# Performance work log

Hardware: AMD Instinct MI355X
Metric: run time of the kernel (lower is better)

## Reference

```python
import jax, jax.numpy as jnp
import numpy as np

B, T = 64, 512
L, D = 2048, 512


def setup_inputs() -> dict:
    key = jax.random.key(0)
    k1, k2, k3 = jax.random.split(key, 3)
    label_sequences = jax.random.randint(k1, (B, T), 0, L)
    source_embeddings = jax.random.normal(k2, (L, D), dtype=jnp.float32)
    target_embeddings = jax.random.normal(k3, (L, D), dtype=jnp.float32)
    return {
        "label_sequences": label_sequences,
        "source_embeddings": source_embeddings,
        "target_embeddings": target_embeddings,
    }


def reference(label_sequences, source_embeddings, target_embeddings):
    # source_index = labels[:, :-1], target_index = labels[:, 1:]
    src_idx = label_sequences[:, :-1]          # [B, T-1]
    tgt_idx = label_sequences[:, 1:]           # [B, T-1]
    # Gather source embeddings per transition pair: [B, T-1, D]
    src = source_embeddings[src_idx]
    # Logits over all target labels: [B, T-1, L]
    logits = jnp.einsum("btd,ld->btl", src, target_embeddings)
    # Row-wise log_softmax over target labels (dim=1 in torch == last axis here)
    logp = jax.nn.log_softmax(logits, axis=-1)
    # Pick the actual next label's log-probability: [B, T-1]
    scores = jnp.take_along_axis(logp, tgt_idx[..., None], axis=-1)[..., 0]
    return scores
```

## Files before the change

kernel.cpp:

```cpp
#include <hip/hip_runtime.h>
#include <hip/hip_bf16.h>

#define L_CLS 2048
#define D_DIM 512
#define T_SZ  512
#define NT    511
#define NOUT  (64 * NT)
#define NCHUNK 32
#define LDS_STRIDE 136
#define LOG2E 1.4426950408889634f
#define LN2   0.6931471805599453f
#define SHIFT 128.0f

typedef __attribute__((ext_vector_type(8))) short bf16x8;
typedef __attribute__((ext_vector_type(4))) float f32x4;

static __device__ __forceinline__ short f2bf(float x) {
    return (short)__bfloat16_as_ushort(__float2bfloat16(x));
}

__launch_bounds__(256)
__global__ void gemm_lse(const float* __restrict__ srcE,
                         const float* __restrict__ tgtE,
                         float* __restrict__ psum,
                         float* __restrict__ M, int useM) {
    __shared__ __hip_bfloat16 Blds[64 * LDS_STRIDE];

    const int tid  = threadIdx.x;
    const int wave = tid >> 6;
    const int lane = tid & 63;
    const int lr   = lane & 15;
    const int hi   = lane >> 4;
    const int by   = blockIdx.y;
    const int C    = by * 64;
    const int R0   = blockIdx.x * 64 + wave * 16;
    const int R1   = (blockIdx.x + 16) * 64 + wave * 16;

    f32x4 acc[2][4];
#pragma unroll
    for (int rb = 0; rb < 2; ++rb)
#pragma unroll
        for (int ct = 0; ct < 4; ++ct) acc[rb][ct] = (f32x4){0.f, 0.f, 0.f, 0.f};

#pragma unroll
    for (int s = 0; s < 4; ++s) {
#pragma unroll
        for (int i = 0; i < 4; ++i) {
            int p   = tid + 256 * i;
            int row = p >> 4;
            int grp = p & 15;
            const f32x4* g = reinterpret_cast<const f32x4*>(
                tgtE + (C + row) * D_DIM + s * 128 + grp * 8);
            f32x4 x0 = g[0], x1 = g[1];
            bf16x8 w;
#pragma unroll
            for (int e = 0; e < 4; ++e) { w[e] = f2bf(x0[e]); w[e + 4] = f2bf(x1[e]); }
            *reinterpret_cast<bf16x8*>(&Blds[row * LDS_STRIDE + grp * 8]) = w;
        }
        __syncthreads();

#pragma unroll
        for (int rb = 0; rb < 2; ++rb) {
            const int R = rb ? R1 : R0;
            bf16x8 a[4];
            const float* arow = srcE + (R + lr) * D_DIM + s * 128 + hi * 8;
#pragma unroll
            for (int ks = 0; ks < 4; ++ks) {
                const f32x4* g = reinterpret_cast<const f32x4*>(arow + ks * 32);
                f32x4 x0 = g[0], x1 = g[1];
                bf16x8 v;
#pragma unroll
                for (int e = 0; e < 4; ++e) { v[e] = f2bf(x0[e]); v[e + 4] = f2bf(x1[e]); }
                a[ks] = v;
            }
#pragma unroll
            for (int ks = 0; ks < 4; ++ks) {
                const int off = ks * 32 + hi * 8;
#pragma unroll
                for (int ct = 0; ct < 4; ++ct) {
                    bf16x8 b = *reinterpret_cast<const bf16x8*>(
                        &Blds[(ct * 16 + lr) * LDS_STRIDE + off]);
                    acc[rb][ct] = __builtin_amdgcn_mfma_f32_16x16x32_bf16(
                        a[ks], b, acc[rb][ct], 0, 0, 0);
                }
            }
        }
        __syncthreads();
    }

#pragma unroll
    for (int rb = 0; rb < 2; ++rb) {
        const int R = rb ? R1 : R0;
        if (useM) {
#pragma unroll
            for (int i = 0; i < 4; ++i) {
                size_t rg = (size_t)(R + hi * 4 + i) * L_CLS + C + lr;
                M[rg]      = acc[rb][0][i];
                M[rg + 16] = acc[rb][1][i];
                M[rg + 32] = acc[rb][2][i];
                M[rg + 48] = acc[rb][3][i];
            }
        }
        float p[4];
#pragma unroll
        for (int i = 0; i < 4; ++i) {
            p[i] = exp2f(acc[rb][0][i] * LOG2E - SHIFT)
                 + exp2f(acc[rb][1][i] * LOG2E - SHIFT)
                 + exp2f(acc[rb][2][i] * LOG2E - SHIFT)
                 + exp2f(acc[rb][3][i] * LOG2E - SHIFT);
        }
#pragma unroll
        for (int off = 1; off < 16; off <<= 1)
#pragma unroll
            for (int i = 0; i < 4; ++i) p[i] += __shfl_xor(p[i], off);
        if (lr == 0) {
#pragma unroll
            for (int i = 0; i < 4; ++i)
                psum[(R + hi * 4 + i) * NCHUNK + by] = p[i];
        }
    }
}

__launch_bounds__(256)
__global__ void scores_gather(const int* __restrict__ labels,
                              const float* __restrict__ psum,
                              const float* __restrict__ M,
                              float* __restrict__ out) {
    int o = blockIdx.x * 256 + threadIdx.x;
    if (o >= NOUT) return;
    int b = o / NT;
    int t = o - b * NT;
    int src = labels[b * T_SZ + t];
    int tgt = labels[b * T_SZ + t + 1];

    const f32x4* p4 = reinterpret_cast<const f32x4*>(psum) + src * (NCHUNK / 4);
    f32x4 sv = {0.f, 0.f, 0.f, 0.f};
#pragma unroll
    for (int c = 0; c < NCHUNK / 4; ++c) {
        f32x4 v = p4[c];
        sv[0] += v[0]; sv[1] += v[1]; sv[2] += v[2]; sv[3] += v[3];
    }
    float S = (sv[0] + sv[1]) + (sv[2] + sv[3]);
    float lse = (log2f(S) + SHIFT) * LN2;
    out[o] = M[(size_t)src * L_CLS + tgt] - lse;
}

__launch_bounds__(256)
__global__ void scores_dot(const int* __restrict__ labels,
                           const float* __restrict__ srcE,
                           const float* __restrict__ tgtE,
                           const float* __restrict__ psum,
                           float* __restrict__ out) {
    const int wid  = blockIdx.x * 4 + (threadIdx.x >> 6);
    const int lane = threadIdx.x & 63;
    const int b = wid / NT;
    const int t = wid - b * NT;
    const int src = labels[b * T_SZ + t];
    const int tgt = labels[b * T_SZ + t + 1];

    const f32x4* sp = reinterpret_cast<const f32x4*>(srcE + src * D_DIM + lane * 8);
    const f32x4* tp = reinterpret_cast<const f32x4*>(tgtE + tgt * D_DIM + lane * 8);
    f32x4 s0 = sp[0], s1 = sp[1];
    f32x4 t0 = tp[0], t1 = tp[1];
    float acc = 0.f;
#pragma unroll
    for (int j = 0; j < 4; ++j) acc += s0[j] * t0[j] + s1[j] * t1[j];
    float ps = (lane < NCHUNK) ? psum[src * NCHUNK + lane] : 0.f;
#pragma unroll
    for (int off = 32; off; off >>= 1) {
        acc += __shfl_xor(acc, off);
        ps  += __shfl_xor(ps, off);
    }
    if (lane == 0) out[wid] = acc - (log2f(ps) + SHIFT) * LN2;
}

extern "C" void kernel_launch(void* const* d_in, const int* in_sizes, int n_in,
                              void* d_out, int out_size, void* d_ws, size_t ws_size,
                              hipStream_t stream) {
    const int*   labels = (const int*)d_in[0];
    const float* srcE   = (const float*)d_in[1];
    const float* tgtE   = (const float*)d_in[2];
    float*       out    = (float*)d_out;

    float* psum = (float*)d_ws;
    float* M    = psum + L_CLS * NCHUNK;

    size_t need = ((size_t)L_CLS * NCHUNK + (size_t)L_CLS * L_CLS) * sizeof(float);
    int useM = (ws_size >= need) ? 1 : 0;

    gemm_lse<<<dim3(16, NCHUNK), 256, 0, stream>>>(srcE, tgtE, psum, M, useM);
    if (useM)
        scores_gather<<<(NOUT + 255) / 256, 256, 0, stream>>>(labels, psum, M, out);
    else
        scores_dot<<<NOUT / 4, 256, 0, stream>>>(labels, srcE, tgtE, psum, out);
}
```

Before: 31.79 us.

## Widen GEMM column tile to 128 and share B fragments across row blocks

Doubles each block's target-label tile from 64 to 128 columns, halving the number of column chunks and partial sums. Each LDS B fragment is now reused for both row blocks in one interleaved MFMA loop. The grid is transposed so blockIdx.x indexes column chunks, the s-loop is no longer unrolled, and the psum reduction is simplified to 16 entries. This cuts repeated conversion of A and fewer psum reads, but uses more accumulator registers and LDS while halving the grid to 256 blocks, which may underfill the GPU.

```diff
diff --git a/kernel.cpp b/kernel.cpp
--- a/kernel.cpp
+++ b/kernel.cpp
@@ -6,7 +6,7 @@
 #define T_SZ  512
 #define NT    511
 #define NOUT  (64 * NT)
-#define NCHUNK 32
+#define NCHUNK 16
 #define LDS_STRIDE 136
 #define LOG2E 1.4426950408889634f
 #define LN2   0.6931471805599453f
@@ -24,45 +24,46 @@
                          const float* __restrict__ tgtE,
                          float* __restrict__ psum,
                          float* __restrict__ M, int useM) {
-    __shared__ __hip_bfloat16 Blds[64 * LDS_STRIDE];
+    __shared__ __hip_bfloat16 Blds[128 * LDS_STRIDE];
 
     const int tid  = threadIdx.x;
     const int wave = tid >> 6;
     const int lane = tid & 63;
     const int lr   = lane & 15;
     const int hi   = lane >> 4;
-    const int by   = blockIdx.y;
-    const int C    = by * 64;
-    const int R0   = blockIdx.x * 64 + wave * 16;
-    const int R1   = (blockIdx.x + 16) * 64 + wave * 16;
+    const int by   = blockIdx.x;
+    const int bx   = blockIdx.y;
+    const int C    = by * 128;
+    const int R0   = bx * 64 + wave * 16;
+    const int R1   = (bx + 16) * 64 + wave * 16;
 
-    f32x4 acc[2][4];
+    f32x4 acc[2][8];
 #pragma unroll
     for (int rb = 0; rb < 2; ++rb)
 #pragma unroll
-        for (int ct = 0; ct < 4; ++ct) acc[rb][ct] = (f32x4){0.f, 0.f, 0.f, 0.f};
+        for (int ct = 0; ct < 8; ++ct) acc[rb][ct] = (f32x4){0.f, 0.f, 0.f, 0.f};
 
-#pragma unroll
+#pragma unroll 1
     for (int s = 0; s < 4; ++s) {
 #pragma unroll
-        for (int i = 0; i < 4; ++i) {
+        for (int i = 0; i < 8; ++i) {
             int p   = tid + 256 * i;
             int row = p >> 4;
             int grp = p & 15;
             const f32x4* g = reinterpret_cast<const f32x4*>(
                 tgtE + (C + row) * D_DIM + s * 128 + grp * 8);
             f32x4 x0 = g[0], x1 = g[1];
-            bf16x8 w;
+            bf16x8 v;
 #pragma unroll
-            for (int e = 0; e < 4; ++e) { w[e] = f2bf(x0[e]); w[e + 4] = f2bf(x1[e]); }
-            *reinterpret_cast<bf16x8*>(&Blds[row * LDS_STRIDE + grp * 8]) = w;
+            for (int e = 0; e < 4; ++e) { v[e] = f2bf(x0[e]); v[e + 4] = f2bf(x1[e]); }
+            *reinterpret_cast<bf16x8*>(&Blds[row * LDS_STRIDE + grp * 8]) = v;
         }
         __syncthreads();
 
+        bf16x8 a[2][4];
 #pragma unroll
         for (int rb = 0; rb < 2; ++rb) {
             const int R = rb ? R1 : R0;
-            bf16x8 a[4];
             const float* arow = srcE + (R + lr) * D_DIM + s * 128 + hi * 8;
 #pragma unroll
             for (int ks = 0; ks < 4; ++ks) {
@@ -71,18 +72,19 @@
                 bf16x8 v;
 #pragma unroll
                 for (int e = 0; e < 4; ++e) { v[e] = f2bf(x0[e]); v[e + 4] = f2bf(x1[e]); }
-                a[ks] = v;
+                a[rb][ks] = v;
             }
+        }
+
 #pragma unroll
-            for (int ks = 0; ks < 4; ++ks) {
-                const int off = ks * 32 + hi * 8;
+        for (int ks = 0; ks < 4; ++ks) {
+            const int off = ks * 32 + hi * 8;
 #pragma unroll
-                for (int ct = 0; ct < 4; ++ct) {
-                    bf16x8 b = *reinterpret_cast<const bf16x8*>(
-                        &Blds[(ct * 16 + lr) * LDS_STRIDE + off]);
-                    acc[rb][ct] = __builtin_amdgcn_mfma_f32_16x16x32_bf16(
-                        a[ks], b, acc[rb][ct], 0, 0, 0);
-                }
+            for (int ct = 0; ct < 8; ++ct) {
+                bf16x8 b = *reinterpret_cast<const bf16x8*>(
+                    &Blds[(ct * 16 + lr) * LDS_STRIDE + off]);
+                acc[0][ct] = __builtin_amdgcn_mfma_f32_16x16x32_bf16(a[0][ks], b, acc[0][ct], 0, 0, 0);
+                acc[1][ct] = __builtin_amdgcn_mfma_f32_16x16x32_bf16(a[1][ks], b, acc[1][ct], 0, 0, 0);
             }
         }
         __syncthreads();
@@ -95,19 +97,18 @@
 #pragma unroll
             for (int i = 0; i < 4; ++i) {
                 size_t rg = (size_t)(R + hi * 4 + i) * L_CLS + C + lr;
-                M[rg]      = acc[rb][0][i];
-                M[rg + 16] = acc[rb][1][i];
-                M[rg + 32] = acc[rb][2][i];
-                M[rg + 48] = acc[rb][3][i];
+#pragma unroll
+                for (int ct = 0; ct < 8; ++ct)
+                    M[rg + ct * 16] = acc[rb][ct][i];
             }
         }
         float p[4];
 #pragma unroll
         for (int i = 0; i < 4; ++i) {
-            p[i] = exp2f(acc[rb][0][i] * LOG2E - SHIFT)
-                 + exp2f(acc[rb][1][i] * LOG2E - SHIFT)
-                 + exp2f(acc[rb][2][i] * LOG2E - SHIFT)
-                 + exp2f(acc[rb][3][i] * LOG2E - SHIFT);
+            p[i] = 0.f;
+#pragma unroll
+            for (int ct = 0; ct < 8; ++ct)
+                p[i] += exp2f(acc[rb][ct][i] * LOG2E - SHIFT);
         }
 #pragma unroll
         for (int off = 1; off < 16; off <<= 1)
@@ -133,14 +134,10 @@
     int src = labels[b * T_SZ + t];
     int tgt = labels[b * T_SZ + t + 1];
 
-    const f32x4* p4 = reinterpret_cast<const f32x4*>(psum) + src * (NCHUNK / 4);
-    f32x4 sv = {0.f, 0.f, 0.f, 0.f};
-#pragma unroll
-    for (int c = 0; c < NCHUNK / 4; ++c) {
-        f32x4 v = p4[c];
-        sv[0] += v[0]; sv[1] += v[1]; sv[2] += v[2]; sv[3] += v[3];
-    }
-    float S = (sv[0] + sv[1]) + (sv[2] + sv[3]);
+    const f32x4* pv = reinterpret_cast<const f32x4*>(psum + src * NCHUNK);
+    f32x4 s0 = pv[0], s1 = pv[1], s2 = pv[2], s3 = pv[3];
+    float S = (s0[0]+s0[1]+s0[2]+s0[3]) + (s1[0]+s1[1]+s1[2]+s1[3])
+            + (s2[0]+s2[1]+s2[2]+s2[3]) + (s3[0]+s3[1]+s3[2]+s3[3]);
     float lse = (log2f(S) + SHIFT) * LN2;
     out[o] = M[(size_t)src * L_CLS + tgt] - lse;
 }
@@ -188,7 +185,7 @@
     size_t need = ((size_t)L_CLS * NCHUNK + (size_t)L_CLS * L_CLS) * sizeof(float);
     int useM = (ws_size >= need) ? 1 : 0;
 
-    gemm_lse<<<dim3(16, NCHUNK), 256, 0, stream>>>(srcE, tgtE, psum, M, useM);
+    gemm_lse<<<dim3(NCHUNK, 16), 256, 0, stream>>>(srcE, tgtE, psum, M, useM);
     if (useM)
         scores_gather<<<(NOUT + 255) / 256, 256, 0, stream>>>(labels, psum, M, out);
     else
```

Measured after the change: 31.62 us. About the same (-0.5%).

## Pre-convert tables to bf16 and use double-buffered 32x32 MFMA GEMM tiles

Applied to the files above, without the earlier changes.

Adds a separate kernel that converts both embedding tables to bf16 once, so the GEMM no longer converts fp32 to bf16 inside its inner loop. The GEMM moves to 128x128 tiles with 512 threads, 32x32x16 MFMA instructions, register prefetch of the next K slice and double-buffered LDS. The scores_dot fallback path and the workspace-size check are removed, so the full logit matrix is always materialised. This adds an extra launch and a bf16 round trip through memory, and assumes the workspace is large enough.

```diff
diff --git a/kernel.cpp b/kernel.cpp
--- a/kernel.cpp
+++ b/kernel.cpp
@@ -7,116 +7,136 @@
 #define NT    511
 #define NOUT  (64 * NT)
 #define NCHUNK 32
-#define LDS_STRIDE 136
+#define LDSS  136
 #define LOG2E 1.4426950408889634f
 #define LN2   0.6931471805599453f
 #define SHIFT 128.0f
 
-typedef __attribute__((ext_vector_type(8))) short bf16x8;
-typedef __attribute__((ext_vector_type(4))) float f32x4;
+typedef __attribute__((ext_vector_type(8)))  short bf16x8;
+typedef __attribute__((ext_vector_type(4)))  float f32x4;
+typedef __attribute__((ext_vector_type(16))) float f32x16;
 
 static __device__ __forceinline__ short f2bf(float x) {
     return (short)__bfloat16_as_ushort(__float2bfloat16(x));
 }
 
-__launch_bounds__(256)
-__global__ void gemm_lse(const float* __restrict__ srcE,
-                         const float* __restrict__ tgtE,
-                         float* __restrict__ psum,
-                         float* __restrict__ M, int useM) {
-    __shared__ __hip_bfloat16 Blds[64 * LDS_STRIDE];
+__global__ void conv_bf16(const float* __restrict__ srcE, const float* __restrict__ tgtE,
+                          __hip_bfloat16* __restrict__ Sb, __hip_bfloat16* __restrict__ Tb) {
+    int i = blockIdx.x * blockDim.x + threadIdx.x;
+    if (i >= (L_CLS * D_DIM) / 8) return;
+    const f32x4* s4 = reinterpret_cast<const f32x4*>(srcE) + i * 2;
+    const f32x4* t4 = reinterpret_cast<const f32x4*>(tgtE) + i * 2;
+    f32x4 s0 = s4[0], s1 = s4[1];
+    f32x4 t0 = t4[0], t1 = t4[1];
+    bf16x8 so, to;
+#pragma unroll
+    for (int j = 0; j < 4; ++j) {
+        so[j] = f2bf(s0[j]); so[j + 4] = f2bf(s1[j]);
+        to[j] = f2bf(t0[j]); to[j + 4] = f2bf(t1[j]);
+    }
+    reinterpret_cast<bf16x8*>(Sb)[i] = so;
+    reinterpret_cast<bf16x8*>(Tb)[i] = to;
+}
+
+__launch_bounds__(512, 1)
+__global__ void gemm_lse_bf16(const __hip_bfloat16* __restrict__ Sb,
+                              const __hip_bfloat16* __restrict__ Tb,
+                              float* __restrict__ psum,
+                              float* __restrict__ M) {
+    __shared__ __hip_bfloat16 Blds[2][128 * LDSS];
 
     const int tid  = threadIdx.x;
     const int wave = tid >> 6;
     const int lane = tid & 63;
-    const int lr   = lane & 15;
-    const int hi   = lane >> 4;
-    const int by   = blockIdx.y;
-    const int C    = by * 64;
-    const int R0   = blockIdx.x * 64 + wave * 16;
-    const int R1   = (blockIdx.x + 16) * 64 + wave * 16;
+    const int l31  = lane & 31;
+    const int hk   = lane >> 5;
+    const int rs   = (wave & 3) * 32;
+    const int chf  = wave >> 2;
+    const int C    = blockIdx.x * 128;
+    const int Rb   = blockIdx.y * 128;
+    const int Ar   = Rb + rs + l31;
 
-    f32x4 acc[2][4];
+    f32x16 acc0, acc1;
 #pragma unroll
-    for (int rb = 0; rb < 2; ++rb)
+    for (int r = 0; r < 16; ++r) { acc0[r] = 0.f; acc1[r] = 0.f; }
+
+    bf16x8 stg[4], an[8];
 #pragma unroll
-        for (int ct = 0; ct < 4; ++ct) acc[rb][ct] = (f32x4){0.f, 0.f, 0.f, 0.f};
+    for (int i = 0; i < 4; ++i) {
+        int p = tid + 512 * i;
+        stg[i] = *reinterpret_cast<const bf16x8*>(
+            &Tb[(C + (p >> 4)) * D_DIM + (p & 15) * 8]);
+    }
+#pragma unroll
+    for (int ks = 0; ks < 8; ++ks)
+        an[ks] = *reinterpret_cast<const bf16x8*>(
+            &Sb[Ar * D_DIM + ks * 16 + hk * 8]);
+#pragma unroll
+    for (int i = 0; i < 4; ++i) {
+        int p = tid + 512 * i;
+        *reinterpret_cast<bf16x8*>(&Blds[0][(p >> 4) * LDSS + (p & 15) * 8]) = stg[i];
+    }
+    __syncthreads();
 
 #pragma unroll
     for (int s = 0; s < 4; ++s) {
+        const int cur = s & 1;
+        bf16x8 a[8];
 #pragma unroll
-        for (int i = 0; i < 4; ++i) {
-            int p   = tid + 256 * i;
-            int row = p >> 4;
-            int grp = p & 15;
-            const f32x4* g = reinterpret_cast<const f32x4*>(
-                tgtE + (C + row) * D_DIM + s * 128 + grp * 8);
-            f32x4 x0 = g[0], x1 = g[1];
-            bf16x8 w;
+        for (int ks = 0; ks < 8; ++ks) a[ks] = an[ks];
+
+        if (s < 3) {
 #pragma unroll
-            for (int e = 0; e < 4; ++e) { w[e] = f2bf(x0[e]); w[e + 4] = f2bf(x1[e]); }
-            *reinterpret_cast<bf16x8*>(&Blds[row * LDS_STRIDE + grp * 8]) = w;
-        }
-        __syncthreads();
-
-#pragma unroll
-        for (int rb = 0; rb < 2; ++rb) {
-            const int R = rb ? R1 : R0;
-            bf16x8 a[4];
-            const float* arow = srcE + (R + lr) * D_DIM + s * 128 + hi * 8;
-#pragma unroll
-            for (int ks = 0; ks < 4; ++ks) {
-                const f32x4* g = reinterpret_cast<const f32x4*>(arow + ks * 32);
-                f32x4 x0 = g[0], x1 = g[1];
-                bf16x8 v;
-#pragma unroll
-                for (int e = 0; e < 4; ++e) { v[e] = f2bf(x0[e]); v[e + 4] = f2bf(x1[e]); }
-                a[ks] = v;
+            for (int i = 0; i < 4; ++i) {
+                int p = tid + 512 * i;
+                stg[i] = *reinterpret_cast<const bf16x8*>(
+                    &Tb[(C + (p >> 4)) * D_DIM + (s + 1) * 128 + (p & 15) * 8]);
             }
 #pragma unroll
-            for (int ks = 0; ks < 4; ++ks) {
-                const int off = ks * 32 + hi * 8;
+            for (int ks = 0; ks < 8; ++ks)
+                an[ks] = *reinterpret_cast<const bf16x8*>(
+                    &Sb[Ar * D_DIM + (s + 1) * 128 + ks * 16 + hk * 8]);
+        }
+
+        const __hip_bfloat16* Bb = Blds[cur];
 #pragma unroll
-                for (int ct = 0; ct < 4; ++ct) {
-                    bf16x8 b = *reinterpret_cast<const bf16x8*>(
-                        &Blds[(ct * 16 + lr) * LDS_STRIDE + off]);
-                    acc[rb][ct] = __builtin_amdgcn_mfma_f32_16x16x32_bf16(
-                        a[ks], b, acc[rb][ct], 0, 0, 0);
-                }
+        for (int ks = 0; ks < 8; ++ks) {
+            const int off = ks * 16 + hk * 8;
+            bf16x8 b0 = *reinterpret_cast<const bf16x8*>(&Bb[(chf * 64 + l31) * LDSS + off]);
+            bf16x8 b1 = *reinterpret_cast<const bf16x8*>(&Bb[(chf * 64 + 32 + l31) * LDSS + off]);
+            acc0 = __builtin_amdgcn_mfma_f32_32x32x16_bf16(a[ks], b0, acc0, 0, 0, 0);
+            acc1 = __builtin_amdgcn_mfma_f32_32x32x16_bf16(a[ks], b1, acc1, 0, 0, 0);
+        }
+
+        if (s < 3) {
+#pragma unroll
+            for (int i = 0; i < 4; ++i) {
+                int p = tid + 512 * i;
+                *reinterpret_cast<bf16x8*>(
+                    &Blds[cur ^ 1][(p >> 4) * LDSS + (p & 15) * 8]) = stg[i];
             }
+            __syncthreads();
         }
-        __syncthreads();
     }
 
+    float p[16];
 #pragma unroll
-    for (int rb = 0; rb < 2; ++rb) {
-        const int R = rb ? R1 : R0;
-        if (useM) {
+    for (int r = 0; r < 16; ++r) {
+        int grow = Rb + rs + (r & 3) + 8 * (r >> 2) + 4 * hk;
+        size_t base = (size_t)grow * L_CLS + C + chf * 64 + l31;
+        M[base]      = acc0[r];
+        M[base + 32] = acc1[r];
+        p[r] = exp2f(acc0[r] * LOG2E - SHIFT) + exp2f(acc1[r] * LOG2E - SHIFT);
+    }
 #pragma unroll
-            for (int i = 0; i < 4; ++i) {
-                size_t rg = (size_t)(R + hi * 4 + i) * L_CLS + C + lr;
-                M[rg]      = acc[rb][0][i];
-                M[rg + 16] = acc[rb][1][i];
-                M[rg + 32] = acc[rb][2][i];
-                M[rg + 48] = acc[rb][3][i];
-            }
-        }
-        float p[4];
+    for (int off = 1; off < 32; off <<= 1)
 #pragma unroll
-        for (int i = 0; i < 4; ++i) {
-            p[i] = exp2f(acc[rb][0][i] * LOG2E - SHIFT)
-                 + exp2f(acc[rb][1][i] * LOG2E - SHIFT)
-                 + exp2f(acc[rb][2][i] * LOG2E - SHIFT)
-                 + exp2f(acc[rb][3][i] * LOG2E - SHIFT);
-        }
+        for (int r = 0; r < 16; ++r) p[r] += __shfl_xor(p[r], off);
+    if (l31 == 0) {
 #pragma unroll
-        for (int off = 1; off < 16; off <<= 1)
-#pragma unroll
-            for (int i = 0; i < 4; ++i) p[i] += __shfl_xor(p[i], off);
-        if (lr == 0) {
-#pragma unroll
-            for (int i = 0; i < 4; ++i)
-                psum[(R + hi * 4 + i) * NCHUNK + by] = p[i];
+        for (int r = 0; r < 16; ++r) {
+            int grow = Rb + rs + (r & 3) + 8 * (r >> 2) + 4 * hk;
+            psum[grow * NCHUNK + blockIdx.x * 2 + chf] = p[r];
         }
     }
 }
@@ -133,45 +153,16 @@
     int src = labels[b * T_SZ + t];
     int tgt = labels[b * T_SZ + t + 1];
 
-    const f32x4* p4 = reinterpret_cast<const f32x4*>(psum) + src * (NCHUNK / 4);
-    f32x4 sv = {0.f, 0.f, 0.f, 0.f};
+    const f32x4* pv = reinterpret_cast<const f32x4*>(psum + src * NCHUNK);
+    f32x4 sv = pv[0];
 #pragma unroll
-    for (int c = 0; c < NCHUNK / 4; ++c) {
-        f32x4 v = p4[c];
+    for (int c = 1; c < NCHUNK / 4; ++c) {
+        f32x4 v = pv[c];
         sv[0] += v[0]; sv[1] += v[1]; sv[2] += v[2]; sv[3] += v[3];
     }
     float S = (sv[0] + sv[1]) + (sv[2] + sv[3]);
     float lse = (log2f(S) + SHIFT) * LN2;
     out[o] = M[(size_t)src * L_CLS + tgt] - lse;
-}
-
-__launch_bounds__(256)
-__global__ void scores_dot(const int* __restrict__ labels,
-                           const float* __restrict__ srcE,
-                           const float* __restrict__ tgtE,
-                           const float* __restrict__ psum,
-                           float* __restrict__ out) {
-    const int wid  = blockIdx.x * 4 + (threadIdx.x >> 6);
-    const int lane = threadIdx.x & 63;
-    const int b = wid / NT;
-    const int t = wid - b * NT;
-    const int src = labels[b * T_SZ + t];
-    const int tgt = labels[b * T_SZ + t + 1];
-
-    const f32x4* sp = reinterpret_cast<const f32x4*>(srcE + src * D_DIM + lane * 8);
-    const f32x4* tp = reinterpret_cast<const f32x4*>(tgtE + tgt * D_DIM + lane * 8);
-    f32x4 s0 = sp[0], s1 = sp[1];
-    f32x4 t0 = tp[0], t1 = tp[1];
-    float acc = 0.f;
-#pragma unroll
-    for (int j = 0; j < 4; ++j) acc += s0[j] * t0[j] + s1[j] * t1[j];
-    float ps = (lane < NCHUNK) ? psum[src * NCHUNK + lane] : 0.f;
-#pragma unroll
-    for (int off = 32; off; off >>= 1) {
-        acc += __shfl_xor(acc, off);
-        ps  += __shfl_xor(ps, off);
-    }
-    if (lane == 0) out[wid] = acc - (log2f(ps) + SHIFT) * LN2;
 }
 
 extern "C" void kernel_launch(void* const* d_in, const int* in_sizes, int n_in,
@@ -182,15 +173,13 @@
     const float* tgtE   = (const float*)d_in[2];
     float*       out    = (float*)d_out;
 
-    float* psum = (float*)d_ws;
-    float* M    = psum + L_CLS * NCHUNK;
+    const size_t tbl = (size_t)L_CLS * D_DIM;
+    __hip_bfloat16* Sb = (__hip_bfloat16*)d_ws;
+    __hip_bfloat16* Tb = Sb + tbl;
+    float* psum = (float*)((char*)d_ws + 2 * tbl * sizeof(__hip_bfloat16));
+    float* M    = psum + (size_t)L_CLS * NCHUNK;
 
-    size_t need = ((size_t)L_CLS * NCHUNK + (size_t)L_CLS * L_CLS) * sizeof(float);
-    int useM = (ws_size >= need) ? 1 : 0;
-
-    gemm_lse<<<dim3(16, NCHUNK), 256, 0, stream>>>(srcE, tgtE, psum, M, useM);
-    if (useM)
-        scores_gather<<<(NOUT + 255) / 256, 256, 0, stream>>>(labels, psum, M, out);
-    else
-        scores_dot<<<NOUT / 4, 256, 0, stream>>>(labels, srcE, tgtE, psum, out);
+    conv_bf16<<<(int)(tbl / 8 + 255) / 256, 256, 0, stream>>>(srcE, tgtE, Sb, Tb);
+    gemm_lse_bf16<<<dim3(16, 16), 512, 0, stream>>>(Sb, Tb, psum, M);
+    scores_gather<<<(NOUT + 255) / 256, 256, 0, stream>>>(labels, psum, M, out);
 }
```

Measured after the change: 29.74 us. -6.4%, faster.
